# Performance work log

Measured on AMD Instinct MI355X. Metric: run time of the kernel, lower is better.

Reference implementation:

```python
import jax, jax.numpy as jnp
import numpy as np

VOCAB, NUM_TAGS, EMB, HID = 30000, 20, 200, 128
B, S = 128, 512


def setup_inputs() -> dict:
    key = jax.random.key(0)
    ks = jax.random.split(key, 13)
    sentence = jax.random.randint(ks[0], (B, S), 0, VOCAB)
    tags = jax.random.randint(ks[1], (B, S), 0, NUM_TAGS)
    lengths = jax.random.randint(ks[2], (B,), 1, S + 1)
    mask = jnp.arange(S)[None, :] < lengths[:, None]  # [B,S] bool, mask[:,0] all True
    sc = 0.1
    return {
        "sentence": sentence,
        "tags": tags,
        "mask": mask,
        "embedding": jax.random.normal(ks[3], (VOCAB, EMB), jnp.float32) * sc,
        "W_ih": jax.random.normal(ks[4], (4 * HID, EMB), jnp.float32) * sc,
        "W_hh": jax.random.normal(ks[5], (4 * HID, HID), jnp.float32) * sc,
        "b_ih": jax.random.normal(ks[6], (4 * HID,), jnp.float32) * sc,
        "b_hh": jax.random.normal(ks[7], (4 * HID,), jnp.float32) * sc,
        "W_dec": jax.random.normal(ks[8], (NUM_TAGS, HID), jnp.float32) * sc,
        "b_dec": jax.random.normal(ks[9], (NUM_TAGS,), jnp.float32) * sc,
        "start_trans": jax.random.normal(ks[10], (NUM_TAGS,), jnp.float32) * sc,
        "end_trans": jax.random.normal(ks[11], (NUM_TAGS,), jnp.float32) * sc,
        "trans": jax.random.normal(ks[12], (NUM_TAGS, NUM_TAGS), jnp.float32) * sc,
    }


def _lstm(embeds, W_ih, W_hh, b_ih, b_hh):
    # torch nn.LSTM, single layer, batch_first, zero init state; gate order i,f,g,o
    b = embeds.shape[0]
    h0 = jnp.zeros((b, HID), embeds.dtype)
    x = jnp.swapaxes(embeds, 0, 1)  # [S,B,E]
    xg = jnp.einsum('sbe,ge->sbg', x, W_ih) + b_ih + b_hh  # input projections, [S,B,4H]

    def step(carry, xg_t):
        h, c = carry
        g = xg_t + h @ W_hh.T
        i, f, gg, o = jnp.split(g, 4, axis=-1)
        c = jax.nn.sigmoid(f) * c + jax.nn.sigmoid(i) * jnp.tanh(gg)
        h = jax.nn.sigmoid(o) * jnp.tanh(c)
        return (h, c), h

    _, hs = jax.lax.scan(step, (h0, h0), xg)
    return jnp.swapaxes(hs, 0, 1)  # [B,S,H]


def _crf_nll_mean(emissions, tags, mask, start_trans, end_trans, trans):
    # torchcrf.CRF negative log likelihood, reduction='mean' (mean over batch)
    b = emissions.shape[0]
    ems = jnp.swapaxes(emissions, 0, 1)          # [S,B,T]
    tgs = jnp.swapaxes(tags, 0, 1)               # [S,B]
    msk = jnp.swapaxes(mask, 0, 1).astype(emissions.dtype)  # [S,B]
    bidx = jnp.arange(b)

    # numerator: score of the gold path
    num0 = start_trans[tgs[0]] + ems[0, bidx, tgs[0]]

    def nstep(score, inp):
        em, tag, ptag, m = inp
        return score + (trans[ptag, tag] + em[bidx, tag]) * m, None

    num, _ = jax.lax.scan(nstep, num0, (ems[1:], tgs[1:], tgs[:-1], msk[1:]))
    last_idx = mask.sum(axis=1).astype(jnp.int32) - 1
    num = num + end_trans[tags[bidx, last_idx]]

    # denominator: forward algorithm (log partition)
    sc0 = start_trans[None, :] + ems[0]  # [B,T]

    def dstep(score, inp):
        em, m = inp
        nxt = jax.nn.logsumexp(score[:, :, None] + trans[None] + em[:, None, :], axis=1)
        return jnp.where(m[:, None] > 0, nxt, score), None

    sc, _ = jax.lax.scan(dstep, sc0, (ems[1:], msk[1:]))
    den = jax.nn.logsumexp(sc + end_trans[None, :], axis=1)
    return -jnp.mean(num - den)


def reference(sentence, tags, mask, embedding, W_ih, W_hh, b_ih, b_hh,
              W_dec, b_dec, start_trans, end_trans, trans):
    embeds = embedding[sentence]                           # [B,S,E]
    lstm_out = _lstm(embeds, W_ih, W_hh, b_ih, b_hh)       # [B,S,H]
    emissions = jnp.einsum('bsh,th->bst', lstm_out, W_dec) + b_dec  # [B,S,T]
    # dropout treated as identity (eval-mode reference)
    return _crf_nll_mean(emissions, tags, mask, start_trans, end_trans, trans)
```

## Files before the change

### kernel.cpp

```cpp
#include <hip/hip_runtime.h>
#include <hip/hip_bf16.h>
#include <hip/hip_fp16.h>
#include <math.h>

#define B_ 128
#define S_ 512
#define EMB_ 200
#define HID_ 128
#define NT_ 20
#define G4_ 512
#define KP_ 224

typedef _Float16 f16x2_t __attribute__((ext_vector_type(2)));
typedef short bf16x8 __attribute__((ext_vector_type(8)));
typedef float f32x4 __attribute__((ext_vector_type(4)));

#if __has_builtin(__builtin_amdgcn_fdot2)
#define FDOT2(a, b, c) __builtin_amdgcn_fdot2(__builtin_bit_cast(f16x2_t, (a)), \
                                              __builtin_bit_cast(f16x2_t, (b)), (c), false)
#else
static __device__ __forceinline__ float fdot2_fb(unsigned a, unsigned b, float c) {
    float alo = __half2float(__ushort_as_half((unsigned short)(a & 0xffffu)));
    float ahi = __half2float(__ushort_as_half((unsigned short)(a >> 16)));
    float blo = __half2float(__ushort_as_half((unsigned short)(b & 0xffffu)));
    float bhi = __half2float(__ushort_as_half((unsigned short)(b >> 16)));
    return c + alo * blo + ahi * bhi;
}
#define FDOT2(a, b, c) fdot2_fb((a), (b), (c))
#endif

__device__ __forceinline__ float bf2f(unsigned u) {
    union { unsigned u; float f; } cv;
    cv.u = u << 16;
    return cv.f;
}
__device__ __forceinline__ unsigned packh2(float a, float b) {
    return ((unsigned)__half_as_ushort(__float2half(b)) << 16)
         | (unsigned)__half_as_ushort(__float2half(a));
}
__device__ __forceinline__ unsigned short f2bf(float f) {
    __hip_bfloat16 h = __float2bfloat16(f);
    unsigned short u;
    __builtin_memcpy(&u, &h, 2);
    return u;
}

__global__ void k_detect(const unsigned char* mask, int* flag) {
    __shared__ int partial[4];
    int tid = threadIdx.x;
    int s = 0;
    for (int i = tid; i < B_ * S_; i += 256) {
        if (i & 3) s += mask[i];
    }
    for (int m = 32; m >= 1; m >>= 1) s += __shfl_xor(s, m);
    if ((tid & 63) == 0) partial[tid >> 6] = s;
    __syncthreads();
    if (tid == 0) {
        int tot = partial[0] + partial[1] + partial[2] + partial[3];
        flag[0] = (tot > 0) ? 1 : 0;
    }
}

__global__ void k_prep(const float* __restrict__ W_ih, const float* __restrict__ b_ih,
                       const float* __restrict__ b_hh, __hip_bfloat16* __restrict__ Wb,
                       float* __restrict__ biasb) {
    int i = blockIdx.x * 256 + threadIdx.x;
    if (i < G4_ * KP_) {
        int g = i / KP_, k = i - g * KP_;
        float v = (k < EMB_) ? W_ih[g * EMB_ + k] : 0.f;
        Wb[i] = __float2bfloat16(v);
    }
    if (i < G4_) biasb[i] = b_ih[i] + b_hh[i];
}

__global__ __launch_bounds__(256, 2) void k_xg(const int* __restrict__ sentence,
                                               const float* __restrict__ embedding,
                                               const __hip_bfloat16* __restrict__ Wb,
                                               const float* __restrict__ biasb,
                                               __hip_bfloat16* __restrict__ xg) {
    __shared__ short Bl[G4_ * 40];
    __shared__ short Al[32 * 40];
    __shared__ int ids_s[32];
    int tid = threadIdx.x;
    int m0 = blockIdx.x * 32;
    int lane = tid & 63;
    int gbase = (tid >> 6) * 128;
    if (tid < 32) ids_s[tid] = sentence[m0 + tid];
    __syncthreads();

    f32x4 acc0[8], acc1[8];
#pragma unroll
    for (int n = 0; n < 8; n++) {
        acc0[n] = (f32x4){0.f, 0.f, 0.f, 0.f};
        acc1[n] = (f32x4){0.f, 0.f, 0.f, 0.f};
    }
    int lrow = lane & 15, lk = lane >> 4;

    for (int c = 0; c < 7; c++) {
        int k0 = c * 32;
#pragma unroll
        for (int i = 0; i < 8; i++) {
            int idx = tid + 256 * i;
            int row = idx >> 2, q = idx & 3;
            uint4 v = *(const uint4*)((const short*)Wb + (size_t)row * KP_ + k0 + q * 8);
            *(uint4*)(Bl + row * 40 + q * 8) = v;
        }
#pragma unroll
        for (int i = 0; i < 2; i++) {
            int j = tid + 256 * i;
            int row = j >> 4, kp = j & 15;
            int k = k0 + kp * 2;
            const float* e = embedding + (size_t)ids_s[row] * EMB_;
            float v0 = (k < EMB_) ? e[k] : 0.f;
            float v1 = (k + 1 < EMB_) ? e[k + 1] : 0.f;
            unsigned u = (unsigned)f2bf(v0) | ((unsigned)f2bf(v1) << 16);
            *(unsigned*)(Al + row * 40 + kp * 2) = u;
        }
        __syncthreads();
        bf16x8 a0 = *(const bf16x8*)(Al + lrow * 40 + lk * 8);
        bf16x8 a1 = *(const bf16x8*)(Al + (lrow + 16) * 40 + lk * 8);
#pragma unroll
        for (int n = 0; n < 8; n++) {
            bf16x8 bfr = *(const bf16x8*)(Bl + (gbase + n * 16 + lrow) * 40 + lk * 8);
            acc0[n] = __builtin_amdgcn_mfma_f32_16x16x32_bf16(a0, bfr, acc0[n], 0, 0, 0);
            acc1[n] = __builtin_amdgcn_mfma_f32_16x16x32_bf16(a1, bfr, acc1[n], 0, 0, 0);
        }
        __syncthreads();
    }
    int rbase = m0 + lk * 4;
#pragma unroll
    for (int n = 0; n < 8; n++) {
        int g = gbase + n * 16 + lrow;
        float bv = biasb[g];
#pragma unroll
        for (int r = 0; r < 4; r++) {
            xg[(size_t)(rbase + r) * G4_ + g] = __float2bfloat16(acc0[n][r] + bv);
            xg[(size_t)(rbase + r + 16) * G4_ + g] = __float2bfloat16(acc1[n][r] + bv);
        }
    }
}

__global__ __launch_bounds__(1024) __attribute__((amdgpu_waves_per_eu(4, 4)))
void k_lstm(const __hip_bfloat16* __restrict__ xg,
            const float* __restrict__ W_hh,
            unsigned* __restrict__ h2_out) {
    __shared__ unsigned h2_lds[64];
    __shared__ float part_lds[G4_];
    __shared__ float gate_lds[G4_];
    int b = blockIdx.x, tid = threadIdx.x;
    int wv = tid >> 6, lane = tid & 63;
    int p = wv >> 3;
    int g = ((wv & 7) << 6) | lane;

    unsigned w2[32];
    const float2* wrow = (const float2*)(W_hh + (size_t)g * HID_ + p * 64);
#pragma unroll
    for (int k = 0; k < 32; k++) {
        float2 f = wrow[k];
        w2[k] = packh2(f.x, f.y);
    }
#pragma unroll
    for (int k = 0; k < 32; k++) asm("" : "+v"(w2[k]));

    if (tid < 64) h2_lds[tid] = 0u;
    float c0 = 0.f, c1 = 0.f;
    const ushort* xgb = (const ushort*)(xg) + (size_t)b * S_ * G4_;
    unsigned* h2b = h2_out + (size_t)b * S_ * 64;
    __syncthreads();

    unsigned xr = (p == 0) ? (unsigned)xgb[g] : 0u;
    for (int t = 0; t < S_; t++) {
        unsigned xr_next = 0u;
        if (p == 0) {
            int tn = (t + 1 < S_) ? t + 1 : t;
            xr_next = xgb[(size_t)tn * G4_ + g];
        }
        float acc = 0.f;
        const uint4* hb4 = (const uint4*)(h2_lds + (p << 5));
#pragma unroll
        for (int q = 0; q < 8; q++) {
            uint4 hh = hb4[q];
            acc = FDOT2(w2[4 * q + 0], hh.x, acc);
            acc = FDOT2(w2[4 * q + 1], hh.y, acc);
            acc = FDOT2(w2[4 * q + 2], hh.z, acc);
            acc = FDOT2(w2[4 * q + 3], hh.w, acc);
        }
        if (p == 1) part_lds[g] = acc;
        __syncthreads();
        if (p == 0) {
            float pre = bf2f(xr) + acc + part_lds[g];
            int gt = g >> 7;
            float xs = (gt == 2) ? 2.f * pre : pre;
            xs = fminf(fmaxf(xs, -30.f), 30.f);
            float r = 1.f / (1.f + __expf(-xs));
            gate_lds[g] = (gt == 2) ? 2.f * r - 1.f : r;
        }
        __syncthreads();
        if (tid < 64) {
            int j = tid;
            float2 iv = *(const float2*)(gate_lds + 2 * j);
            float2 fv = *(const float2*)(gate_lds + 128 + 2 * j);
            float2 gv = *(const float2*)(gate_lds + 256 + 2 * j);
            float2 ov = *(const float2*)(gate_lds + 384 + 2 * j);
            c0 = fv.x * c0 + iv.x * gv.x;
            c1 = fv.y * c1 + iv.y * gv.y;
            float h0 = ov.x * (2.f / (1.f + __expf(-2.f * c0)) - 1.f);
            float h1 = ov.y * (2.f / (1.f + __expf(-2.f * c1)) - 1.f);
            unsigned pk = packh2(h0, h1);
            h2_lds[j] = pk;
            h2b[(size_t)t * 64 + j] = pk;
        }
        __syncthreads();
        xr = xr_next;
    }
}

__global__ __launch_bounds__(320) void k_em(const unsigned* __restrict__ h2,
                                            const float* __restrict__ W_dec,
                                            const float* __restrict__ b_dec,
                                            float* __restrict__ em) {
    int half = threadIdx.x / 160;
    int r = threadIdx.x % 160;
    int tag = r >> 3, l8 = r & 7;
    const float* wd = W_dec + tag * HID_ + l8 * 16;
    float ws[16];
#pragma unroll
    for (int q = 0; q < 16; q++) ws[q] = wd[q];
    float bd = b_dec[tag];
    int row0 = blockIdx.x * 16 + half * 8;
    for (int rp = 0; rp < 8; rp++) {
        int row = row0 + rp;
        const uint4* h4 = (const uint4*)(h2 + (size_t)row * 64 + l8 * 8);
        uint4 a = h4[0], bq = h4[1];
        unsigned hv[8] = {a.x, a.y, a.z, a.w, bq.x, bq.y, bq.z, bq.w};
        float pacc = 0.f;
#pragma unroll
        for (int q = 0; q < 8; q++) {
            float lo = __half2float(__ushort_as_half((unsigned short)(hv[q] & 0xffffu)));
            float hi = __half2float(__ushort_as_half((unsigned short)(hv[q] >> 16)));
            pacc += lo * ws[2 * q] + hi * ws[2 * q + 1];
        }
        pacc += __shfl_xor(pacc, 1);
        pacc += __shfl_xor(pacc, 2);
        pacc += __shfl_xor(pacc, 4);
        if (l8 == 0) em[(size_t)row * NT_ + tag] = pacc + bd;
    }
}

__global__ __launch_bounds__(64) void k_crf(const float* __restrict__ em,
                                            const int* __restrict__ tags,
                                            const void* __restrict__ mask,
                                            const int* __restrict__ flag,
                                            const float* __restrict__ start_trans,
                                            const float* __restrict__ end_trans,
                                            const float* __restrict__ trans,
                                            float* __restrict__ nll) {
    __shared__ float em_s[S_ * NT_];
    __shared__ float trans_s[NT_ * NT_];
    __shared__ int tags_s[S_];
    __shared__ unsigned char mask_s[S_];
    __shared__ __align__(16) float score_s[32];
    __shared__ float num_sh;

    int b = blockIdx.x;
    int lane = threadIdx.x;
    const float4* e4 = (const float4*)(em + (size_t)b * S_ * NT_);
    float4* s4 = (float4*)em_s;
    for (int i = lane; i < S_ * NT_ / 4; i += 64) s4[i] = e4[i];
    for (int i = lane; i < NT_ * NT_; i += 64) trans_s[i] = trans[i];
    for (int i = lane; i < S_; i += 64) tags_s[i] = tags[b * S_ + i];
    int fl = flag[0];
    for (int i = lane; i < S_; i += 64) {
        mask_s[i] = fl ? ((const unsigned char*)mask)[b * S_ + i]
                       : (unsigned char)(((const int*)mask)[b * S_ + i] != 0);
    }
    __syncthreads();

    float nsum = 0.f;
    int cnt = 0;
    for (int t = lane; t < S_; t += 64) cnt += mask_s[t];
    for (int t = 1 + lane; t < S_; t += 64) {
        if (mask_s[t]) {
            int tg = tags_s[t], pt = tags_s[t - 1];
            nsum += trans_s[pt * NT_ + tg] + em_s[t * NT_ + tg];
        }
    }
    for (int m = 32; m >= 1; m >>= 1) {
        nsum += __shfl_xor(nsum, m);
        cnt += __shfl_xor(cnt, m);
    }
    if (lane == 0) {
        int t0 = tags_s[0];
        num_sh = nsum + start_trans[t0] + em_s[t0] + end_trans[tags_s[cnt - 1]];
    }

    int tag = (lane < NT_) ? lane : NT_ - 1;
    float tcol[NT_];
#pragma unroll
    for (int p = 0; p < NT_; p++) tcol[p] = trans_s[p * NT_ + tag];
    float sc = start_trans[tag] + em_s[tag];
    if (lane < NT_) score_s[lane] = sc;
    __syncthreads();

    for (int t = 1; t < S_; t++) {
        const float4* q4 = (const float4*)score_s;
        float4 q0 = q4[0], q1 = q4[1], q2 = q4[2], q3 = q4[3], q5 = q4[4];
        float v[NT_] = {q0.x + tcol[0],  q0.y + tcol[1],  q0.z + tcol[2],  q0.w + tcol[3],
                        q1.x + tcol[4],  q1.y + tcol[5],  q1.z + tcol[6],  q1.w + tcol[7],
                        q2.x + tcol[8],  q2.y + tcol[9],  q2.z + tcol[10], q2.w + tcol[11],
                        q3.x + tcol[12], q3.y + tcol[13], q3.z + tcol[14], q3.w + tcol[15],
                        q5.x + tcol[16], q5.y + tcol[17], q5.z + tcol[18], q5.w + tcol[19]};
        float mx[NT_];
#pragma unroll
        for (int p = 0; p < NT_; p++) mx[p] = v[p];
#pragma unroll
        for (int n = NT_; n > 1; n = (n + 1) >> 1) {
#pragma unroll
            for (int i = 0; i < (n >> 1); i++) mx[i] = fmaxf(mx[i], mx[n - 1 - i]);
        }
        float ex[NT_];
#pragma unroll
        for (int p = 0; p < NT_; p++) ex[p] = __expf(v[p] - mx[0]);
#pragma unroll
        for (int n = NT_; n > 1; n = (n + 1) >> 1) {
#pragma unroll
            for (int i = 0; i < (n >> 1); i++) ex[i] += ex[n - 1 - i];
        }
        float nxt = mx[0] + __logf(ex[0]) + em_s[t * NT_ + tag];
        sc = mask_s[t] ? nxt : sc;
        __syncthreads();
        if (lane < NT_) score_s[lane] = sc;
        __syncthreads();
    }

    if (lane < NT_) score_s[lane] = sc + end_trans[tag];
    __syncthreads();
    if (lane == 0) {
        float m = score_s[0];
#pragma unroll
        for (int i = 1; i < NT_; i++) m = fmaxf(m, score_s[i]);
        float s = 0.f;
#pragma unroll
        for (int i = 0; i < NT_; i++) s += __expf(score_s[i] - m);
        nll[b] = (m + __logf(s)) - num_sh;
    }
}

__global__ void k_final(const float* __restrict__ nll, float* __restrict__ out) {
    __shared__ float sums[2];
    int tid = threadIdx.x;
    float v = nll[tid];
    for (int m = 32; m >= 1; m >>= 1) v += __shfl_xor(v, m);
    if ((tid & 63) == 0) sums[tid >> 6] = v;
    __syncthreads();
    if (tid == 0) out[0] = (sums[0] + sums[1]) * (1.f / (float)B_);
}

extern "C" void kernel_launch(void* const* d_in, const int* in_sizes, int n_in,
                              void* d_out, int out_size, void* d_ws, size_t ws_size,
                              hipStream_t stream) {
    const int* sentence = (const int*)d_in[0];
    const int* tags = (const int*)d_in[1];
    const void* mask = d_in[2];
    const float* embedding = (const float*)d_in[3];
    const float* W_ih = (const float*)d_in[4];
    const float* W_hh = (const float*)d_in[5];
    const float* b_ih = (const float*)d_in[6];
    const float* b_hh = (const float*)d_in[7];
    const float* W_dec = (const float*)d_in[8];
    const float* b_dec = (const float*)d_in[9];
    const float* start_trans = (const float*)d_in[10];
    const float* end_trans = (const float*)d_in[11];
    const float* trans = (const float*)d_in[12];

    char* ws = (char*)d_ws;
    int* flag = (int*)ws;
    __hip_bfloat16* xg = (__hip_bfloat16*)(ws + 256);
    size_t off = 256 + (size_t)B_ * S_ * G4_ * 2;
    float* em = (float*)(ws + off);
    off += (size_t)B_ * S_ * NT_ * 4;
    float* nllp = (float*)(ws + off);
    off += 512;
    unsigned* h2_out = (unsigned*)(ws + off);
    off += (size_t)B_ * S_ * 64 * 4;
    __hip_bfloat16* Wb = (__hip_bfloat16*)(ws + off);
    off += (size_t)G4_ * KP_ * 2;
    float* biasb = (float*)(ws + off);

    k_detect<<<1, 256, 0, stream>>>((const unsigned char*)mask, flag);
    k_prep<<<(G4_ * KP_ + 255) / 256, 256, 0, stream>>>(W_ih, b_ih, b_hh, Wb, biasb);
    k_xg<<<(B_ * S_) / 32, 256, 0, stream>>>(sentence, embedding, Wb, biasb, xg);
    k_lstm<<<B_, 1024, 0, stream>>>(xg, W_hh, h2_out);
    k_em<<<(B_ * S_) / 16, 320, 0, stream>>>(h2_out, W_dec, b_dec, em);
    k_crf<<<B_, 64, 0, stream>>>(em, tags, mask, flag, start_trans, end_trans, trans, nllp);
    k_final<<<1, 128, 0, stream>>>(nllp, (float*)d_out);
}
```

Before: 709.9 us.

## Fuse emission projection into LSTM, merge detect into prep, drop CRF barriers

Folds the mask-detect kernel into the prep kernel as an extra block and packs W_dec to fp16 pairs there. The emission decoder is moved to the tail of the LSTM kernel and uses fdot2 with W_dec held in LDS, which removes the separate k_em launch. k_xg now gathers whole embedding rows once before its K loop, and the CRF loop drops its __syncthreads because it runs as a single wavefront. These changes cut launch overhead and redundant passes, but the fused decoder tail runs on only 128 blocks and leaves a serial per-row loop.

New measurement: 716.3 us. No clear change (+0.9%).

```diff
diff --git a/kernel.cpp b/kernel.cpp
--- a/kernel.cpp
+++ b/kernel.cpp
@@ -45,25 +45,26 @@
     return u;
 }
 
-__global__ void k_detect(const unsigned char* mask, int* flag) {
-    __shared__ int partial[4];
-    int tid = threadIdx.x;
-    int s = 0;
-    for (int i = tid; i < B_ * S_; i += 256) {
-        if (i & 3) s += mask[i];
-    }
-    for (int m = 32; m >= 1; m >>= 1) s += __shfl_xor(s, m);
-    if ((tid & 63) == 0) partial[tid >> 6] = s;
-    __syncthreads();
-    if (tid == 0) {
-        int tot = partial[0] + partial[1] + partial[2] + partial[3];
-        flag[0] = (tot > 0) ? 1 : 0;
-    }
-}
-
 __global__ void k_prep(const float* __restrict__ W_ih, const float* __restrict__ b_ih,
-                       const float* __restrict__ b_hh, __hip_bfloat16* __restrict__ Wb,
-                       float* __restrict__ biasb) {
+                       const float* __restrict__ b_hh, const float* __restrict__ W_dec,
+                       const unsigned char* __restrict__ mask,
+                       __hip_bfloat16* __restrict__ Wb, float* __restrict__ biasb,
+                       unsigned* __restrict__ Wd2, int* __restrict__ flag) {
+    if (blockIdx.x == 448) {
+        __shared__ int partial[4];
+        int tid = threadIdx.x;
+        int s = 0;
+        for (int i = tid; i < B_ * S_; i += 256) {
+            if (i & 3) s += mask[i];
+        }
+        for (int m = 32; m >= 1; m >>= 1) s += __shfl_xor(s, m);
+        if ((tid & 63) == 0) partial[tid >> 6] = s;
+        __syncthreads();
+        if (tid == 0) {
+            flag[0] = ((partial[0] + partial[1] + partial[2] + partial[3]) > 0) ? 1 : 0;
+        }
+        return;
+    }
     int i = blockIdx.x * 256 + threadIdx.x;
     if (i < G4_ * KP_) {
         int g = i / KP_, k = i - g * KP_;
@@ -71,6 +72,10 @@
         Wb[i] = __float2bfloat16(v);
     }
     if (i < G4_) biasb[i] = b_ih[i] + b_hh[i];
+    if (i < NT_ * 64) {
+        int tg = i >> 6, j = i & 63;
+        Wd2[i] = packh2(W_dec[tg * HID_ + 2 * j], W_dec[tg * HID_ + 2 * j + 1]);
+    }
 }
 
 __global__ __launch_bounds__(256, 2) void k_xg(const int* __restrict__ sentence,
@@ -79,7 +84,7 @@
                                                const float* __restrict__ biasb,
                                                __hip_bfloat16* __restrict__ xg) {
     __shared__ short Bl[G4_ * 40];
-    __shared__ short Al[32 * 40];
+    __shared__ short Al[32 * 232];
     __shared__ int ids_s[32];
     int tid = threadIdx.x;
     int m0 = blockIdx.x * 32;
@@ -88,6 +93,17 @@
     if (tid < 32) ids_s[tid] = sentence[m0 + tid];
     __syncthreads();
 
+    for (int i = tid; i < 32 * 112; i += 256) {
+        int row = i / 112, kp = i - row * 112;
+        int k = kp * 2;
+        unsigned u = 0u;
+        if (k < EMB_) {
+            float2 v = *(const float2*)(embedding + (size_t)ids_s[row] * EMB_ + k);
+            u = (unsigned)f2bf(v.x) | ((unsigned)f2bf(v.y) << 16);
+        }
+        *(unsigned*)(Al + row * 232 + k) = u;
+    }
+
     f32x4 acc0[8], acc1[8];
 #pragma unroll
     for (int n = 0; n < 8; n++) {
@@ -105,20 +121,9 @@
             uint4 v = *(const uint4*)((const short*)Wb + (size_t)row * KP_ + k0 + q * 8);
             *(uint4*)(Bl + row * 40 + q * 8) = v;
         }
-#pragma unroll
-        for (int i = 0; i < 2; i++) {
-            int j = tid + 256 * i;
-            int row = j >> 4, kp = j & 15;
-            int k = k0 + kp * 2;
-            const float* e = embedding + (size_t)ids_s[row] * EMB_;
-            float v0 = (k < EMB_) ? e[k] : 0.f;
-            float v1 = (k + 1 < EMB_) ? e[k + 1] : 0.f;
-            unsigned u = (unsigned)f2bf(v0) | ((unsigned)f2bf(v1) << 16);
-            *(unsigned*)(Al + row * 40 + kp * 2) = u;
-        }
-        __syncthreads();
-        bf16x8 a0 = *(const bf16x8*)(Al + lrow * 40 + lk * 8);
-        bf16x8 a1 = *(const bf16x8*)(Al + (lrow + 16) * 40 + lk * 8);
+        __syncthreads();
+        bf16x8 a0 = *(const bf16x8*)(Al + lrow * 232 + k0 + lk * 8);
+        bf16x8 a1 = *(const bf16x8*)(Al + (lrow + 16) * 232 + k0 + lk * 8);
 #pragma unroll
         for (int n = 0; n < 8; n++) {
             bf16x8 bfr = *(const bf16x8*)(Bl + (gbase + n * 16 + lrow) * 40 + lk * 8);
@@ -143,10 +148,15 @@
 __global__ __launch_bounds__(1024) __attribute__((amdgpu_waves_per_eu(4, 4)))
 void k_lstm(const __hip_bfloat16* __restrict__ xg,
             const float* __restrict__ W_hh,
-            unsigned* __restrict__ h2_out) {
+            const unsigned* __restrict__ Wd2,
+            const float* __restrict__ b_dec,
+            unsigned* __restrict__ h2_out,
+            float* __restrict__ em) {
     __shared__ unsigned h2_lds[64];
     __shared__ float part_lds[G4_];
     __shared__ float gate_lds[G4_];
+    __shared__ unsigned wd_lds[NT_ * 64];
+    __shared__ float bd_lds[NT_];
     int b = blockIdx.x, tid = threadIdx.x;
     int wv = tid >> 6, lane = tid & 63;
     int p = wv >> 3;
@@ -162,6 +172,8 @@
 #pragma unroll
     for (int k = 0; k < 32; k++) asm("" : "+v"(w2[k]));
 
+    for (int i = tid; i < NT_ * 64; i += 1024) wd_lds[i] = Wd2[i];
+    if (tid < NT_) bd_lds[tid] = b_dec[tid];
     if (tid < 64) h2_lds[tid] = 0u;
     float c0 = 0.f, c1 = 0.f;
     const ushort* xgb = (const ushort*)(xg) + (size_t)b * S_ * G4_;
@@ -213,37 +225,28 @@
         __syncthreads();
         xr = xr_next;
     }
-}
-
-__global__ __launch_bounds__(320) void k_em(const unsigned* __restrict__ h2,
-                                            const float* __restrict__ W_dec,
-                                            const float* __restrict__ b_dec,
-                                            float* __restrict__ em) {
-    int half = threadIdx.x / 160;
-    int r = threadIdx.x % 160;
-    int tag = r >> 3, l8 = r & 7;
-    const float* wd = W_dec + tag * HID_ + l8 * 16;
-    float ws[16];
-#pragma unroll
-    for (int q = 0; q < 16; q++) ws[q] = wd[q];
-    float bd = b_dec[tag];
-    int row0 = blockIdx.x * 16 + half * 8;
-    for (int rp = 0; rp < 8; rp++) {
-        int row = row0 + rp;
-        const uint4* h4 = (const uint4*)(h2 + (size_t)row * 64 + l8 * 8);
-        uint4 a = h4[0], bq = h4[1];
-        unsigned hv[8] = {a.x, a.y, a.z, a.w, bq.x, bq.y, bq.z, bq.w};
-        float pacc = 0.f;
-#pragma unroll
-        for (int q = 0; q < 8; q++) {
-            float lo = __half2float(__ushort_as_half((unsigned short)(hv[q] & 0xffffu)));
-            float hi = __half2float(__ushort_as_half((unsigned short)(hv[q] >> 16)));
-            pacc += lo * ws[2 * q] + hi * ws[2 * q + 1];
-        }
-        pacc += __shfl_xor(pacc, 1);
-        pacc += __shfl_xor(pacc, 2);
-        pacc += __shfl_xor(pacc, 4);
-        if (l8 == 0) em[(size_t)row * NT_ + tag] = pacc + bd;
+
+    __syncthreads();
+    if (tid < 512) {
+        int r = tid;
+        const uint4* hp = (const uint4*)(h2b + (size_t)r * 64);
+        uint4 hrow[16];
+#pragma unroll
+        for (int q = 0; q < 16; q++) hrow[q] = hp[q];
+        float* emr = em + (size_t)b * S_ * NT_ + (size_t)r * NT_;
+        for (int tg = 0; tg < NT_; tg++) {
+            const uint4* wd4 = (const uint4*)(wd_lds + tg * 64);
+            float a = 0.f;
+#pragma unroll
+            for (int q = 0; q < 16; q++) {
+                uint4 w4 = wd4[q];
+                a = FDOT2(w4.x, hrow[q].x, a);
+                a = FDOT2(w4.y, hrow[q].y, a);
+                a = FDOT2(w4.z, hrow[q].z, a);
+                a = FDOT2(w4.w, hrow[q].w, a);
+            }
+            emr[tg] = a + bd_lds[tg];
+        }
     }
 }
 
@@ -300,7 +303,6 @@
     for (int p = 0; p < NT_; p++) tcol[p] = trans_s[p * NT_ + tag];
     float sc = start_trans[tag] + em_s[tag];
     if (lane < NT_) score_s[lane] = sc;
-    __syncthreads();
 
     for (int t = 1; t < S_; t++) {
         const float4* q4 = (const float4*)score_s;
@@ -328,9 +330,7 @@
         }
         float nxt = mx[0] + __logf(ex[0]) + em_s[t * NT_ + tag];
         sc = mask_s[t] ? nxt : sc;
-        __syncthreads();
         if (lane < NT_) score_s[lane] = sc;
-        __syncthreads();
     }
 
     if (lane < NT_) score_s[lane] = sc + end_trans[tag];
@@ -386,12 +386,13 @@
     __hip_bfloat16* Wb = (__hip_bfloat16*)(ws + off);
     off += (size_t)G4_ * KP_ * 2;
     float* biasb = (float*)(ws + off);
-
-    k_detect<<<1, 256, 0, stream>>>((const unsigned char*)mask, flag);
-    k_prep<<<(G4_ * KP_ + 255) / 256, 256, 0, stream>>>(W_ih, b_ih, b_hh, Wb, biasb);
+    off += 2048;
+    unsigned* Wd2 = (unsigned*)(ws + off);
+
+    k_prep<<<449, 256, 0, stream>>>(W_ih, b_ih, b_hh, W_dec,
+                                    (const unsigned char*)mask, Wb, biasb, Wd2, flag);
     k_xg<<<(B_ * S_) / 32, 256, 0, stream>>>(sentence, embedding, Wb, biasb, xg);
-    k_lstm<<<B_, 1024, 0, stream>>>(xg, W_hh, h2_out);
-    k_em<<<(B_ * S_) / 16, 320, 0, stream>>>(h2_out, W_dec, b_dec, em);
+    k_lstm<<<B_, 1024, 0, stream>>>(xg, W_hh, Wd2, b_dec, h2_out, em);
     k_crf<<<B_, 64, 0, stream>>>(em, tags, mask, flag, start_trans, end_trans, trans, nllp);
     k_final<<<1, 128, 0, stream>>>(nllp, (float*)d_out);
 }
```
